# Performance work log

Hardware: AMD Instinct MI355X
Metric: run time of the kernel (lower is better)

## Reference

```python
import jax, jax.numpy as jnp
import numpy as np

B, C, H, W = 4, 256, 64, 64
RC = 32  # reduced channels = C // reduction


def setup_inputs() -> dict:
    key = jax.random.key(0)
    ks = jax.random.split(key, 5)
    return {
        "x": jax.random.normal(ks[0], (B, C, H, W), dtype=jnp.float32),
        "context": jax.random.normal(ks[1], (B, C, H, W), dtype=jnp.float32),
        "Wq": jax.random.normal(ks[2], (RC, C), dtype=jnp.float32) * 0.02,
        "bq": jnp.zeros((RC,), dtype=jnp.float32),
        "Wk": jax.random.normal(ks[3], (RC, C), dtype=jnp.float32) * 0.02,
        "bk": jnp.zeros((RC,), dtype=jnp.float32),
        "Wv": jax.random.normal(ks[4], (C, C), dtype=jnp.float32) * 0.02,
        "bv": jnp.zeros((C,), dtype=jnp.float32),
        "gamma": jnp.ones((1,), dtype=jnp.float32),
    }


def reference(x, context, Wq, bq, Wk, bk, Wv, bv, gamma):
    b, c, h, w = x.shape
    _, _, hc, wc = context.shape
    n, m = h * w, hc * wc
    xf = x.reshape(b, c, n)          # (B,C,N)
    cf = context.reshape(b, c, m)    # (B,C,M)
    # 1x1 conv projections == per-pixel linear
    q = jnp.einsum('rc,bcn->bnr', Wq, xf) + bq            # (B,N,RC)
    k = jnp.einsum('rc,bcm->brm', Wk, cf) + bk[:, None]   # (B,RC,M)
    v = jnp.einsum('dc,bcm->bdm', Wv, cf) + bv[:, None]   # (B,C,M)
    scale = 1.0 / jnp.sqrt(jnp.asarray(q.shape[-1], dtype=q.dtype))
    attn = jax.nn.softmax(jnp.einsum('bnr,brm->bnm', q, k) * scale, axis=-1)  # (B,N,M)
    out = jnp.einsum('bdm,bnm->bdn', v, attn).reshape(b, c, h, w)
    return gamma * out + x
```

## Files before the change

### kernel.cpp

```cpp
#include <hip/hip_runtime.h>
#include <hip/hip_bf16.h>


#define B_ 4
#define C_ 256
#define N_ 4096
#define M_ 4096
#define SCALE_ 0.17677669529663687f

typedef __bf16 bf16x8 __attribute__((ext_vector_type(8)));
typedef float f32x4 __attribute__((ext_vector_type(4)));
typedef float f32x16 __attribute__((ext_vector_type(16)));
typedef int i32x8 __attribute__((ext_vector_type(8)));

#define AS1 __attribute__((address_space(1)))
#define AS3 __attribute__((address_space(3)))

static __device__ __forceinline__ unsigned short f2bf(float f) {
    unsigned int u = __float_as_uint(f);
    return (unsigned short)((u + 0x7fffu + ((u >> 16) & 1u)) >> 16);
}
static __device__ __forceinline__ unsigned bfpk(float a, float b) {
    return (unsigned)f2bf(a) | ((unsigned)f2bf(b) << 16);
}

__global__ __launch_bounds__(256) void prep(
        const float* __restrict__ Wq, const float* __restrict__ Wk,
        const float* __restrict__ Wv, uint4* __restrict__ Wqf,
        uint4* __restrict__ Wkf, uint4* __restrict__ Wvf) {
    int bid = blockIdx.x, t = threadIdx.x;
    const float* W;
    uint4* dst;
    int frag;
    if (bid < 32)      { W = Wv; dst = Wvf; frag = (bid * 256 + t) >> 6; }
    else if (bid < 36) { W = Wq; dst = Wqf; frag = ((bid - 32) * 256 + t) >> 6; }
    else               { W = Wk; dst = Wkf; frag = ((bid - 36) * 256 + t) >> 6; }
    int lane = t & 63, low = lane & 15, q = lane >> 4;
    int fch = frag & 7, fr = frag >> 3;
    const float* wp = W + (size_t)(fr * 16 + low) * C_ + fch * 32 + q * 8;
    float4 w0 = *(const float4*)wp;
    float4 w1 = *(const float4*)(wp + 4);
    uint4 pk = {bfpk(w0.x, w0.y), bfpk(w0.z, w0.w),
                bfpk(w1.x, w1.y), bfpk(w1.z, w1.w)};
    dst[(size_t)frag * 64 + lane] = pk;
}

__global__ __launch_bounds__(256, 2) void fused_proj(
        const float* __restrict__ x, const float* __restrict__ ctx,
        const uint4* __restrict__ Wqf, const uint4* __restrict__ Wkf,
        const uint4* __restrict__ Wvf,
        const float* __restrict__ bq, const float* __restrict__ bk,
        const float* __restrict__ bv,
        unsigned short* __restrict__ Qf, unsigned short* __restrict__ Kf,
        unsigned char* __restrict__ Vf) {
    __shared__ unsigned short X[64][264];
    __shared__ unsigned short Pl[4][16 * 40];
    __shared__ unsigned char  Vw[4][16 * 40];

    int bid = blockIdx.x;
    bool isX = bid >= 256;
    int lb = bid & 255;
    int b = lb >> 6, pt64 = lb & 63;
    const float* __restrict__ in = (isX ? x : ctx) + (size_t)b * C_ * N_ + pt64 * 64;
    int t = threadIdx.x, wg = t >> 6, lane = t & 63;
    int low = lane & 15, q = lane >> 4;

    {
        int pL = lane;
        const float* s0 = in + pL;
#pragma unroll
        for (int ct = 0; ct < 4; ct++) {
            const float* s2 = s0 + (size_t)(ct * 64 + wg * 16) * N_;
            float v[16];
#pragma unroll
            for (int k = 0; k < 16; k++) v[k] = s2[(size_t)k * N_];
#pragma unroll
            for (int k = 0; k < 16; k += 2)
                *(unsigned*)&X[pL][ct * 64 + wg * 16 + k] = bfpk(v[k], v[k + 1]);
        }
    }
    __syncthreads();

    {
        const uint4* __restrict__ Wf = isX ? Wqf : Wkf;
        const float* __restrict__ bias = isX ? bq : bk;
        unsigned short* __restrict__ dst = isX ? Qf : Kf;
        bf16x8 xf[8];
#pragma unroll
        for (int ch = 0; ch < 8; ch++)
            xf[ch] = *(const bf16x8*)&X[wg * 16 + low][ch * 32 + q * 8];
        const f32x4 zero = {0.f, 0.f, 0.f, 0.f};
        f32x4 acc[2] = {zero, zero};
#pragma unroll
        for (int rt = 0; rt < 2; rt++)
#pragma unroll
            for (int ch = 0; ch < 8; ch++) {
                uint4 wv = Wf[(rt * 8 + ch) * 64 + lane];
                acc[rt] = __builtin_amdgcn_mfma_f32_16x16x32_bf16(
                    __builtin_bit_cast(bf16x8, wv), xf[ch], acc[rt], 0, 0, 0);
            }
        unsigned short* Pw = &Pl[wg][0];
#pragma unroll
        for (int rt = 0; rt < 2; rt++) {
            float b0 = bias[rt * 16 + q * 4 + 0], b1 = bias[rt * 16 + q * 4 + 1];
            float b2 = bias[rt * 16 + q * 4 + 2], b3 = bias[rt * 16 + q * 4 + 3];
            uint2 pk = {bfpk(acc[rt][0] + b0, acc[rt][1] + b1),
                        bfpk(acc[rt][2] + b2, acc[rt][3] + b3)};
            *(uint2*)(Pw + low * 40 + rt * 16 + q * 4) = pk;
        }
        uint4 frag = *(const uint4*)(Pw + low * 40 + q * 8);
        ((uint4*)dst)[((size_t)b * 256 + pt64 * 4 + wg) * 64 + lane] = frag;
    }

    if (!isX) {
        int mstep = wg >> 1, dh = wg & 1;
        bf16x8 vfr[2][8];
#pragma unroll
        for (int mt = 0; mt < 2; mt++)
#pragma unroll
            for (int ch = 0; ch < 8; ch++)
                vfr[mt][ch] = *(const bf16x8*)&X[mstep * 32 + mt * 16 + low][ch * 32 + q * 8];
        unsigned char* Vv = &Vw[wg][0];
        int msg = pt64 * 2 + mstep;
        const f32x4 zero = {0.f, 0.f, 0.f, 0.f};
#pragma unroll
        for (int dt8 = 0; dt8 < 8; dt8++) {
            int dt = dh * 8 + dt8;
            f32x4 a0 = zero, a1 = zero;
#pragma unroll
            for (int ch = 0; ch < 8; ch++) {
                uint4 wv = Wvf[(dt * 8 + ch) * 64 + lane];
                bf16x8 wfr = __builtin_bit_cast(bf16x8, wv);
                a0 = __builtin_amdgcn_mfma_f32_16x16x32_bf16(vfr[0][ch], wfr, a0, 0, 0, 0);
                a1 = __builtin_amdgcn_mfma_f32_16x16x32_bf16(vfr[1][ch], wfr, a1, 0, 0, 0);
            }
            float bb = bv[dt * 16 + low];
            unsigned w0 = __builtin_amdgcn_cvt_pk_fp8_f32(a0[0] + bb, a0[1] + bb, 0, false);
            w0 = __builtin_amdgcn_cvt_pk_fp8_f32(a0[2] + bb, a0[3] + bb, w0, true);
            unsigned w1 = __builtin_amdgcn_cvt_pk_fp8_f32(a1[0] + bb, a1[1] + bb, 0, false);
            w1 = __builtin_amdgcn_cvt_pk_fp8_f32(a1[2] + bb, a1[3] + bb, w1, true);
            *(unsigned*)(Vv + low * 40 + q * 4) = w0;
            *(unsigned*)(Vv + low * 40 + 16 + q * 4) = w1;
            uint2 fr = *(const uint2*)(Vv + low * 40 + q * 8);
            ((uint2*)Vf)[(((size_t)b * 128 + msg) * 16 + dt) * 64 + lane] = fr;
        }
    }
}

__global__ __launch_bounds__(512, 2) void attn(
        const unsigned short* __restrict__ Qf, const unsigned short* __restrict__ Kf,
        const unsigned char* __restrict__ Vf, const float* __restrict__ x,
        const float* __restrict__ gamma, float* __restrict__ out) {
    __shared__ __align__(16) unsigned char Pb[2][4][16 * 80];
    __shared__ float l_sh[64];
    __shared__ unsigned Ot[64 * 129];

    int bid = blockIdx.x;
    int xcd = bid & 7, tq = bid >> 3;
    int b = xcd >> 1;
    int g = ((xcd & 1) << 5) + tq;

    int wave = threadIdx.x >> 6, lane = threadIdx.x & 63;
    int q = lane >> 4, low = lane & 15;
    int hi = lane >> 5;
    int dsel = q & 1;
    int l31 = lane & 31;
    bool isQK = wave < 4;

    const uint4* Qp = (const uint4*)Qf;
    const uint4* Kp = (const uint4*)Kf + (size_t)b * 256 * 64;
    const uint2* Vq = (const uint2*)(Vf + (size_t)b * 1048576) + (size_t)hi * 1024 + low;
    int dt = wave * 2 + dsel;

    bf16x8 qa;
    if (isQK)
        qa = __builtin_bit_cast(bf16x8, Qp[(size_t)(b * 256 + g * 4 + wave) * 64 + lane]);

    f32x16 acc2[2];
    acc2[0] = (f32x16)(0.f);
    acc2[1] = (f32x16)(0.f);
    float lacc = 0.f;
    const f32x4 zero = {0.f, 0.f, 0.f, 0.f};

    uint4 kv[4];
    f32x4 s[4];
    if (isQK) {
#pragma unroll
        for (int u = 0; u < 4; u++)
            kv[u] = Kp[(size_t)u * 64 + lane];
#pragma unroll
        for (int u = 0; u < 4; u++)
            s[u] = __builtin_amdgcn_mfma_f32_16x16x32_bf16(
                __builtin_bit_cast(bf16x8, kv[u]), qa, zero, 0, 0, 0);
#pragma unroll
        for (int u = 0; u < 4; u++)
            kv[u] = Kp[(size_t)(4 + u) * 64 + lane];
        unsigned char* Pw = &Pb[0][wave][0];
#pragma unroll
        for (int u = 0; u < 4; u++) {
            float p0 = __expf(s[u][0] * SCALE_), p1 = __expf(s[u][1] * SCALE_);
            float p2 = __expf(s[u][2] * SCALE_), p3 = __expf(s[u][3] * SCALE_);
            lacc += p0 + p1 + p2 + p3;
            unsigned w = __builtin_amdgcn_cvt_pk_fp8_f32(p0, p1, 0, false);
            w = __builtin_amdgcn_cvt_pk_fp8_f32(p2, p3, w, true);
            *(unsigned*)(Pw + low * 80 + u * 16 + q * 4) = w;
        }
    }
    i32x8 vfc;
    {
        const uint2* Vs = Vq + (size_t)dt * 64;
        long* dqw = (long*)&vfc;
#pragma unroll
        for (int ss = 0; ss < 4; ss++)
            dqw[ss] = *(const long*)(Vs + ss * 16);
    }
    __syncthreads();

    for (int i = 0; i < 64; i++) {
        int cur = i & 1, nxt = cur ^ 1;
        bool haveNext = (i + 1 < 64);

        i32x8 vfn;
        if (haveNext) {
            const uint2* Vs = Vq + (size_t)(i + 1) * 2048 + dt * 64;
            long* dqw = (long*)&vfn;
#pragma unroll
            for (int ss = 0; ss < 4; ss++)
                dqw[ss] = *(const long*)(Vs + ss * 16);
        }

        if (isQK && haveNext) {
#pragma unroll
            for (int u = 0; u < 4; u++)
                s[u] = __builtin_amdgcn_mfma_f32_16x16x32_bf16(
                    __builtin_bit_cast(bf16x8, kv[u]), qa, zero, 0, 0, 0);
            if (i + 2 < 64) {
#pragma unroll
                for (int u = 0; u < 4; u++)
                    kv[u] = Kp[(size_t)((i + 2) * 4 + u) * 64 + lane];
            }
        }

        const unsigned char* Pr = &Pb[cur][0][0];
        __builtin_amdgcn_s_setprio(1);
#pragma unroll
        for (int tp = 0; tp < 2; tp++) {
            const unsigned char* pr = Pr + (tp * 2 + dsel) * 1280 + low * 80 + hi * 32;
            i32x8 pf;
            ((uint4*)&pf)[0] = *(const uint4*)pr;
            ((uint4*)&pf)[1] = *(const uint4*)(pr + 16);
            acc2[tp] = __builtin_amdgcn_mfma_scale_f32_32x32x64_f8f6f4(
                vfc, pf, acc2[tp], 0, 0, 0, 127, 0, 127);
        }
        __builtin_amdgcn_s_setprio(0);

        if (isQK && haveNext) {
            unsigned char* Pw = &Pb[nxt][wave][0];
#pragma unroll
            for (int u = 0; u < 4; u++) {
                float p0 = __expf(s[u][0] * SCALE_), p1 = __expf(s[u][1] * SCALE_);
                float p2 = __expf(s[u][2] * SCALE_), p3 = __expf(s[u][3] * SCALE_);
                lacc += p0 + p1 + p2 + p3;
                unsigned w = __builtin_amdgcn_cvt_pk_fp8_f32(p0, p1, 0, false);
                w = __builtin_amdgcn_cvt_pk_fp8_f32(p2, p3, w, true);
                *(unsigned*)(Pw + low * 80 + u * 16 + q * 4) = w;
            }
        }
        if (haveNext) vfc = vfn;
        __syncthreads();
    }

    if (isQK) {
        lacc += __shfl_xor(lacc, 16, 64);
        lacc += __shfl_xor(lacc, 32, 64);
        if (lane < 16)
            l_sh[wave * 16 + low] = lacc;
    }

#pragma unroll
    for (int tp = 0; tp < 2; tp++)
#pragma unroll
        for (int r = 0; r < 16; r += 2) {
            int col16 = wave * 16 + ((r >> 1) & 1) + 4 * (r >> 2) + 2 * hi;
            Ot[(tp * 32 + l31) * 129 + col16] = bfpk(acc2[tp][r], acc2[tp][r + 1]);
        }
    __syncthreads();

    {
        float gm = gamma[0];
        float rinv = gm / l_sh[lane];
        size_t nb = ((size_t)(b * 256 + wave * 32)) * 4096 + g * 64 + lane;
#pragma unroll 4
        for (int j = 0; j < 32; j++) {
            unsigned pk = Ot[lane * 129 + wave * 16 + (j >> 1)];
            unsigned bits = (j & 1) ? (pk & 0xffff0000u) : (pk << 16);
            float o = __uint_as_float(bits);
            size_t idx = nb + (size_t)j * 4096;
            out[idx] = o * rinv + x[idx];
        }
    }
}

extern "C" void kernel_launch(void* const* d_in, const int* in_sizes, int n_in,
                              void* d_out, int out_size, void* d_ws, size_t ws_size,
                              hipStream_t stream) {
    const float* x     = (const float*)d_in[0];
    const float* ctx   = (const float*)d_in[1];
    const float* Wq    = (const float*)d_in[2];
    const float* bq    = (const float*)d_in[3];
    const float* Wk    = (const float*)d_in[4];
    const float* bk    = (const float*)d_in[5];
    const float* Wv    = (const float*)d_in[6];
    const float* bv    = (const float*)d_in[7];
    const float* gamma = (const float*)d_in[8];
    float* out = (float*)d_out;

    unsigned short* Qf = (unsigned short*)d_ws;
    unsigned short* Kf = Qf + (size_t)B_ * N_ * 32;
    unsigned char*  Vf = (unsigned char*)(Kf + (size_t)B_ * M_ * 32);
    uint4* Wqf = (uint4*)(Vf + (size_t)B_ * M_ * C_);
    uint4* Wkf = Wqf + 16 * 64;
    uint4* Wvf = Wkf + 16 * 64;

    prep<<<40, 256, 0, stream>>>(Wq, Wk, Wv, Wqf, Wkf, Wvf);
    fused_proj<<<512, 256, 0, stream>>>(x, ctx, Wqf, Wkf, Wvf, bq, bk, bv, Qf, Kf, Vf);
    attn<<<256, 512, 0, stream>>>(Qf, Kf, Vf, x, gamma, out);
}
```

Before: 139.6 us.

## Halve attention query tile per block, double grid, use lighter barrier

Each attention block now handles 32 query rows instead of 64, so twice as many blocks are launched and launch bounds allow 4 blocks per CU. The QK work is split so that four waves each compute half the keys for one of two 16-query tiles, and the row sums are combined from two partial sums. A custom barrier waits only on LDS counters instead of using a full __syncthreads. The aim is better occupancy and latency hiding across 256 CUs, at the cost of reloading every V fragment twice as often overall and doing less MFMA work per barrier.

After: 142.2 us. Within noise of the previous version (+1.9%).

```diff
diff --git a/kernel.cpp b/kernel.cpp
--- a/kernel.cpp
+++ b/kernel.cpp
@@ -22,6 +22,11 @@
 }
 static __device__ __forceinline__ unsigned bfpk(float a, float b) {
     return (unsigned)f2bf(a) | ((unsigned)f2bf(b) << 16);
+}
+static __device__ __forceinline__ void p_barrier() {
+    asm volatile("s_waitcnt lgkmcnt(0)" ::: "memory");
+    __builtin_amdgcn_s_barrier();
+    asm volatile("" ::: "memory");
 }
 
 __global__ __launch_bounds__(256) void prep(
@@ -147,18 +152,18 @@
     }
 }
 
-__global__ __launch_bounds__(512, 2) void attn(
+__global__ __launch_bounds__(512, 4) void attn(
         const unsigned short* __restrict__ Qf, const unsigned short* __restrict__ Kf,
         const unsigned char* __restrict__ Vf, const float* __restrict__ x,
         const float* __restrict__ gamma, float* __restrict__ out) {
-    __shared__ __align__(16) unsigned char Pb[2][4][16 * 80];
-    __shared__ float l_sh[64];
-    __shared__ unsigned Ot[64 * 129];
+    __shared__ __align__(16) unsigned char Pb[2][2][16 * 80];
+    __shared__ float l_sh[2][32];
+    __shared__ unsigned Ot[32 * 129];
 
     int bid = blockIdx.x;
-    int xcd = bid & 7, tq = bid >> 3;
+    int xcd = bid & 7;
     int b = xcd >> 1;
-    int g = ((xcd & 1) << 5) + tq;
+    int g = ((xcd & 1) << 6) | (bid >> 3);
 
     int wave = threadIdx.x >> 6, lane = threadIdx.x & 63;
     int q = lane >> 4, low = lane & 15;
@@ -166,6 +171,8 @@
     int dsel = q & 1;
     int l31 = lane & 31;
     bool isQK = wave < 4;
+    int t = wave & 1;
+    int h = (wave >> 1) & 1;
 
     const uint4* Qp = (const uint4*)Qf;
     const uint4* Kp = (const uint4*)Kf + (size_t)b * 256 * 64;
@@ -174,36 +181,34 @@
 
     bf16x8 qa;
     if (isQK)
-        qa = __builtin_bit_cast(bf16x8, Qp[(size_t)(b * 256 + g * 4 + wave) * 64 + lane]);
-
-    f32x16 acc2[2];
-    acc2[0] = (f32x16)(0.f);
-    acc2[1] = (f32x16)(0.f);
+        qa = __builtin_bit_cast(bf16x8, Qp[(size_t)(b * 256 + g * 2 + t) * 64 + lane]);
+
+    f32x16 acc = (f32x16)(0.f);
     float lacc = 0.f;
     const f32x4 zero = {0.f, 0.f, 0.f, 0.f};
 
-    uint4 kv[4];
-    f32x4 s[4];
+    uint4 kv[2];
+    f32x4 s[2];
     if (isQK) {
 #pragma unroll
-        for (int u = 0; u < 4; u++)
-            kv[u] = Kp[(size_t)u * 64 + lane];
-#pragma unroll
-        for (int u = 0; u < 4; u++)
+        for (int u = 0; u < 2; u++)
+            kv[u] = Kp[(size_t)(h * 2 + u) * 64 + lane];
+#pragma unroll
+        for (int u = 0; u < 2; u++)
             s[u] = __builtin_amdgcn_mfma_f32_16x16x32_bf16(
                 __builtin_bit_cast(bf16x8, kv[u]), qa, zero, 0, 0, 0);
 #pragma unroll
-        for (int u = 0; u < 4; u++)
-            kv[u] = Kp[(size_t)(4 + u) * 64 + lane];
-        unsigned char* Pw = &Pb[0][wave][0];
-#pragma unroll
-        for (int u = 0; u < 4; u++) {
+        for (int u = 0; u < 2; u++)
+            kv[u] = Kp[(size_t)(4 + h * 2 + u) * 64 + lane];
+        unsigned char* Pw = &Pb[0][t][0];
+#pragma unroll
+        for (int u = 0; u < 2; u++) {
             float p0 = __expf(s[u][0] * SCALE_), p1 = __expf(s[u][1] * SCALE_);
             float p2 = __expf(s[u][2] * SCALE_), p3 = __expf(s[u][3] * SCALE_);
             lacc += p0 + p1 + p2 + p3;
             unsigned w = __builtin_amdgcn_cvt_pk_fp8_f32(p0, p1, 0, false);
             w = __builtin_amdgcn_cvt_pk_fp8_f32(p2, p3, w, true);
-            *(unsigned*)(Pw + low * 80 + u * 16 + q * 4) = w;
+            *(unsigned*)(Pw + low * 80 + h * 32 + u * 16 + q * 4) = w;
         }
     }
     i32x8 vfc;
@@ -214,7 +219,7 @@
         for (int ss = 0; ss < 4; ss++)
             dqw[ss] = *(const long*)(Vs + ss * 16);
     }
-    __syncthreads();
+    p_barrier();
 
     for (int i = 0; i < 64; i++) {
         int cur = i & 1, nxt = cur ^ 1;
@@ -231,68 +236,66 @@
 
         if (isQK && haveNext) {
 #pragma unroll
-            for (int u = 0; u < 4; u++)
+            for (int u = 0; u < 2; u++)
                 s[u] = __builtin_amdgcn_mfma_f32_16x16x32_bf16(
                     __builtin_bit_cast(bf16x8, kv[u]), qa, zero, 0, 0, 0);
             if (i + 2 < 64) {
 #pragma unroll
-                for (int u = 0; u < 4; u++)
-                    kv[u] = Kp[(size_t)((i + 2) * 4 + u) * 64 + lane];
+                for (int u = 0; u < 2; u++)
+                    kv[u] = Kp[(size_t)((i + 2) * 4 + h * 2 + u) * 64 + lane];
             }
         }
 
-        const unsigned char* Pr = &Pb[cur][0][0];
-        __builtin_amdgcn_s_setprio(1);
-#pragma unroll
-        for (int tp = 0; tp < 2; tp++) {
-            const unsigned char* pr = Pr + (tp * 2 + dsel) * 1280 + low * 80 + hi * 32;
+        {
+            const unsigned char* pr = &Pb[cur][0][0] + dsel * 1280 + low * 80 + hi * 32;
             i32x8 pf;
             ((uint4*)&pf)[0] = *(const uint4*)pr;
             ((uint4*)&pf)[1] = *(const uint4*)(pr + 16);
-            acc2[tp] = __builtin_amdgcn_mfma_scale_f32_32x32x64_f8f6f4(
-                vfc, pf, acc2[tp], 0, 0, 0, 127, 0, 127);
-        }
-        __builtin_amdgcn_s_setprio(0);
+            __builtin_amdgcn_s_setprio(1);
+            acc = __builtin_amdgcn_mfma_scale_f32_32x32x64_f8f6f4(
+                vfc, pf, acc, 0, 0, 0, 127, 0, 127);
+            __builtin_amdgcn_s_setprio(0);
+        }
 
         if (isQK && haveNext) {
-            unsigned char* Pw = &Pb[nxt][wave][0];
-#pragma unroll
-            for (int u = 0; u < 4; u++) {
+            unsigned char* Pw = &Pb[nxt][t][0];
+#pragma unroll
+            for (int u = 0; u < 2; u++) {
                 float p0 = __expf(s[u][0] * SCALE_), p1 = __expf(s[u][1] * SCALE_);
                 float p2 = __expf(s[u][2] * SCALE_), p3 = __expf(s[u][3] * SCALE_);
                 lacc += p0 + p1 + p2 + p3;
                 unsigned w = __builtin_amdgcn_cvt_pk_fp8_f32(p0, p1, 0, false);
                 w = __builtin_amdgcn_cvt_pk_fp8_f32(p2, p3, w, true);
-                *(unsigned*)(Pw + low * 80 + u * 16 + q * 4) = w;
+                *(unsigned*)(Pw + low * 80 + h * 32 + u * 16 + q * 4) = w;
             }
         }
         if (haveNext) vfc = vfn;
-        __syncthreads();
+        p_barrier();
     }
 
     if (isQK) {
         lacc += __shfl_xor(lacc, 16, 64);
         lacc += __shfl_xor(lacc, 32, 64);
         if (lane < 16)
-            l_sh[wave * 16 + low] = lacc;
-    }
-
-#pragma unroll
-    for (int tp = 0; tp < 2; tp++)
-#pragma unroll
-        for (int r = 0; r < 16; r += 2) {
-            int col16 = wave * 16 + ((r >> 1) & 1) + 4 * (r >> 2) + 2 * hi;
-            Ot[(tp * 32 + l31) * 129 + col16] = bfpk(acc2[tp][r], acc2[tp][r + 1]);
-        }
+            l_sh[h][t * 16 + low] = lacc;
+    }
+
+#pragma unroll
+    for (int r = 0; r < 16; r += 2) {
+        int col16 = wave * 16 + ((r >> 1) & 1) + 4 * (r >> 2) + 2 * hi;
+        Ot[l31 * 129 + col16] = bfpk(acc[r], acc[r + 1]);
+    }
     __syncthreads();
 
     {
         float gm = gamma[0];
-        float rinv = gm / l_sh[lane];
-        size_t nb = ((size_t)(b * 256 + wave * 32)) * 4096 + g * 64 + lane;
+        float rinv = gm / (l_sh[0][l31] + l_sh[1][l31]);
+        int dh = lane >> 5;
+        size_t nb = ((size_t)(b * 256 + wave * 32 + dh * 16)) * 4096
+                    + (size_t)g * 32 + l31;
 #pragma unroll 4
-        for (int j = 0; j < 32; j++) {
-            unsigned pk = Ot[lane * 129 + wave * 16 + (j >> 1)];
+        for (int j = 0; j < 16; j++) {
+            unsigned pk = Ot[l31 * 129 + wave * 16 + dh * 8 + (j >> 1)];
             unsigned bits = (j & 1) ? (pk & 0xffff0000u) : (pk << 16);
             float o = __uint_as_float(bits);
             size_t idx = nb + (size_t)j * 4096;
@@ -324,5 +327,5 @@
 
     prep<<<40, 256, 0, stream>>>(Wq, Wk, Wv, Wqf, Wkf, Wvf);
     fused_proj<<<512, 256, 0, stream>>>(x, ctx, Wqf, Wkf, Wvf, bq, bk, bv, Qf, Kf, Vf);
-    attn<<<256, 512, 0, stream>>>(Qf, Kf, Vf, x, gamma, out);
-}
+    attn<<<512, 512, 0, stream>>>(Qf, Kf, Vf, x, gamma, out);
+}
```

## Stream K tiles into LDS asynchronously and use contiguous V fragment loads

Applied to the files above, without the earlier changes.

K tiles are now prefetched with global_load_lds directly into a double-buffered LDS area two iterations ahead, and the QK waves read them from LDS rather than holding them in registers. The V fragment layout written by the prep kernel is permuted so each lane's 32-byte V fragment is contiguous and can be loaded with a single vector load. The __syncthreads is replaced by a manual vmcnt wait plus s_barrier so outstanding V loads can stay in flight across the barrier. The aim is to cut register pressure and global load latency in the attention loop, at the cost of relying on hand-placed waitcnt counts being correct.

Result: slower. 152.1 us (+9.0%).

```diff
diff --git a/kernel.cpp b/kernel.cpp
--- a/kernel.cpp
+++ b/kernel.cpp
@@ -22,6 +22,15 @@
 }
 static __device__ __forceinline__ unsigned bfpk(float a, float b) {
     return (unsigned)f2bf(a) | ((unsigned)f2bf(b) << 16);
+}
+static __device__ __forceinline__ void gload_lds16(const void* g, void* l) {
+    __builtin_amdgcn_global_load_lds((const AS1 unsigned int*)g,
+                                     (AS3 unsigned int*)l, 16, 0, 0);
+}
+static __device__ __forceinline__ void p_barrier() {
+    asm volatile("s_waitcnt lgkmcnt(0)" ::: "memory");
+    __builtin_amdgcn_s_barrier();
+    asm volatile("" ::: "memory");
 }
 
 __global__ __launch_bounds__(256) void prep(
@@ -122,6 +131,7 @@
                 vfr[mt][ch] = *(const bf16x8*)&X[mstep * 32 + mt * 16 + low][ch * 32 + q * 8];
         unsigned char* Vv = &Vw[wg][0];
         int msg = pt64 * 2 + mstep;
+        int perm = (lane & 15) * 4 + (lane >> 4);
         const f32x4 zero = {0.f, 0.f, 0.f, 0.f};
 #pragma unroll
         for (int dt8 = 0; dt8 < 8; dt8++) {
@@ -142,7 +152,7 @@
             *(unsigned*)(Vv + low * 40 + q * 4) = w0;
             *(unsigned*)(Vv + low * 40 + 16 + q * 4) = w1;
             uint2 fr = *(const uint2*)(Vv + low * 40 + q * 8);
-            ((uint2*)Vf)[(((size_t)b * 128 + msg) * 16 + dt) * 64 + lane] = fr;
+            ((uint2*)Vf)[(((size_t)b * 128 + msg) * 16 + dt) * 64 + perm] = fr;
         }
     }
 }
@@ -152,6 +162,7 @@
         const unsigned char* __restrict__ Vf, const float* __restrict__ x,
         const float* __restrict__ gamma, float* __restrict__ out) {
     __shared__ __align__(16) unsigned char Pb[2][4][16 * 80];
+    __shared__ __align__(16) unsigned char Kl[2][4096];
     __shared__ float l_sh[64];
     __shared__ unsigned Ot[64 * 129];
 
@@ -168,9 +179,11 @@
     bool isQK = wave < 4;
 
     const uint4* Qp = (const uint4*)Qf;
-    const uint4* Kp = (const uint4*)Kf + (size_t)b * 256 * 64;
-    const uint2* Vq = (const uint2*)(Vf + (size_t)b * 1048576) + (size_t)hi * 1024 + low;
+    const unsigned char* Kb = (const unsigned char*)(Kf + (size_t)b * 256 * 32 * 2 * 4);
+    Kb = (const unsigned char*)Kf + (size_t)b * 262144;
     int dt = wave * 2 + dsel;
+    const unsigned char* Vq = Vf + (size_t)b * 1048576
+                              + (size_t)hi * 8192 + (size_t)dt * 512 + (size_t)low * 32;
 
     bf16x8 qa;
     if (isQK)
@@ -187,14 +200,17 @@
     if (isQK) {
 #pragma unroll
         for (int u = 0; u < 4; u++)
-            kv[u] = Kp[(size_t)u * 64 + lane];
+            kv[u] = *(const uint4*)(Kb + (size_t)(u * 64 + lane) * 16);
+        gload_lds16(Kb + 4096 + wave * 1024 + lane * 16,
+                    &Kl[0][wave * 1024 + lane * 16]);
+    }
+    asm volatile("" ::: "memory");
+    i32x8 vfc = *(const i32x8*)Vq;
+    if (isQK) {
 #pragma unroll
         for (int u = 0; u < 4; u++)
             s[u] = __builtin_amdgcn_mfma_f32_16x16x32_bf16(
                 __builtin_bit_cast(bf16x8, kv[u]), qa, zero, 0, 0, 0);
-#pragma unroll
-        for (int u = 0; u < 4; u++)
-            kv[u] = Kp[(size_t)(4 + u) * 64 + lane];
         unsigned char* Pw = &Pb[0][wave][0];
 #pragma unroll
         for (int u = 0; u < 4; u++) {
@@ -206,39 +222,29 @@
             *(unsigned*)(Pw + low * 80 + u * 16 + q * 4) = w;
         }
     }
-    i32x8 vfc;
-    {
-        const uint2* Vs = Vq + (size_t)dt * 64;
-        long* dqw = (long*)&vfc;
-#pragma unroll
-        for (int ss = 0; ss < 4; ss++)
-            dqw[ss] = *(const long*)(Vs + ss * 16);
-    }
-    __syncthreads();
+    asm volatile("s_waitcnt vmcnt(2)" ::: "memory");
+    p_barrier();
 
     for (int i = 0; i < 64; i++) {
         int cur = i & 1, nxt = cur ^ 1;
-        bool haveNext = (i + 1 < 64);
+        bool hn = (i + 1 < 64);
+
+        if (isQK && i + 2 < 64)
+            gload_lds16(Kb + (size_t)(i + 2) * 4096 + wave * 1024 + lane * 16,
+                        &Kl[nxt][wave * 1024 + lane * 16]);
+        asm volatile("" ::: "memory");
 
         i32x8 vfn;
-        if (haveNext) {
-            const uint2* Vs = Vq + (size_t)(i + 1) * 2048 + dt * 64;
-            long* dqw = (long*)&vfn;
-#pragma unroll
-            for (int ss = 0; ss < 4; ss++)
-                dqw[ss] = *(const long*)(Vs + ss * 16);
-        }
-
-        if (isQK && haveNext) {
+        if (hn) vfn = *(const i32x8*)(Vq + (size_t)(i + 1) * 16384);
+
+        if (isQK && hn) {
+#pragma unroll
+            for (int u = 0; u < 4; u++)
+                kv[u] = *(const uint4*)&Kl[cur][u * 1024 + lane * 16];
 #pragma unroll
             for (int u = 0; u < 4; u++)
                 s[u] = __builtin_amdgcn_mfma_f32_16x16x32_bf16(
                     __builtin_bit_cast(bf16x8, kv[u]), qa, zero, 0, 0, 0);
-            if (i + 2 < 64) {
-#pragma unroll
-                for (int u = 0; u < 4; u++)
-                    kv[u] = Kp[(size_t)((i + 2) * 4 + u) * 64 + lane];
-            }
         }
 
         const unsigned char* Pr = &Pb[cur][0][0];
@@ -254,7 +260,7 @@
         }
         __builtin_amdgcn_s_setprio(0);
 
-        if (isQK && haveNext) {
+        if (isQK && hn) {
             unsigned char* Pw = &Pb[nxt][wave][0];
 #pragma unroll
             for (int u = 0; u < 4; u++) {
@@ -266,8 +272,9 @@
                 *(unsigned*)(Pw + low * 80 + u * 16 + q * 4) = w;
             }
         }
-        if (haveNext) vfc = vfn;
-        __syncthreads();
+        if (hn) vfc = vfn;
+        asm volatile("s_waitcnt vmcnt(2)" ::: "memory");
+        p_barrier();
     }
 
     if (isQK) {
```

## Double-buffer V fragments two steps ahead and use a barrier that skips the vmcnt wait

Applied to the files above, without the earlier changes.

The main loop now prefetches V fragments two iterations ahead into two alternating register sets (vA/vB), unrolled by two. The exp/P-write work for the next tile moves ahead of the PV MFMAs. __syncthreads is replaced with a barrier that waits only on LDS counters (lgkmcnt), so global V and K loads stay in flight across barriers. The aim is to hide global-load latency and stop barriers from draining vmcnt, at the cost of more registers and a subtler ordering that relies on the P double buffer.

Result: slower. 147.9 us (+6.0%).

```diff
diff --git a/kernel.cpp b/kernel.cpp
--- a/kernel.cpp
+++ b/kernel.cpp
@@ -22,6 +22,11 @@
 }
 static __device__ __forceinline__ unsigned bfpk(float a, float b) {
     return (unsigned)f2bf(a) | ((unsigned)f2bf(b) << 16);
+}
+static __device__ __forceinline__ void p_barrier() {
+    asm volatile("s_waitcnt lgkmcnt(0)" ::: "memory");
+    __builtin_amdgcn_s_barrier();
+    asm volatile("" ::: "memory");
 }
 
 __global__ __launch_bounds__(256) void prep(
@@ -184,6 +189,18 @@
 
     uint4 kv[4];
     f32x4 s[4];
+    i32x8 vA, vB;
+
+    {
+        long* dqw = (long*)&vA;
+#pragma unroll
+        for (int ss = 0; ss < 4; ss++)
+            dqw[ss] = *(const long*)(Vq + dt * 64 + ss * 16);
+        long* dqx = (long*)&vB;
+#pragma unroll
+        for (int ss = 0; ss < 4; ss++)
+            dqx[ss] = *(const long*)(Vq + 2048 + dt * 64 + ss * 16);
+    }
     if (isQK) {
 #pragma unroll
         for (int u = 0; u < 4; u++)
@@ -206,56 +223,20 @@
             *(unsigned*)(Pw + low * 80 + u * 16 + q * 4) = w;
         }
     }
-    i32x8 vfc;
-    {
-        const uint2* Vs = Vq + (size_t)dt * 64;
-        long* dqw = (long*)&vfc;
-#pragma unroll
-        for (int ss = 0; ss < 4; ss++)
-            dqw[ss] = *(const long*)(Vs + ss * 16);
-    }
-    __syncthreads();
-
-    for (int i = 0; i < 64; i++) {
-        int cur = i & 1, nxt = cur ^ 1;
-        bool haveNext = (i + 1 < 64);
-
-        i32x8 vfn;
-        if (haveNext) {
-            const uint2* Vs = Vq + (size_t)(i + 1) * 2048 + dt * 64;
-            long* dqw = (long*)&vfn;
-#pragma unroll
-            for (int ss = 0; ss < 4; ss++)
-                dqw[ss] = *(const long*)(Vs + ss * 16);
-        }
-
-        if (isQK && haveNext) {
+    p_barrier();
+
+    auto step = [&](int j, i32x8& Vuse) {
+        if (isQK && j + 1 < 64) {
 #pragma unroll
             for (int u = 0; u < 4; u++)
                 s[u] = __builtin_amdgcn_mfma_f32_16x16x32_bf16(
                     __builtin_bit_cast(bf16x8, kv[u]), qa, zero, 0, 0, 0);
-            if (i + 2 < 64) {
+            if (j + 2 < 64) {
 #pragma unroll
                 for (int u = 0; u < 4; u++)
-                    kv[u] = Kp[(size_t)((i + 2) * 4 + u) * 64 + lane];
-            }
-        }
-
-        const unsigned char* Pr = &Pb[cur][0][0];
-        __builtin_amdgcn_s_setprio(1);
-#pragma unroll
-        for (int tp = 0; tp < 2; tp++) {
-            const unsigned char* pr = Pr + (tp * 2 + dsel) * 1280 + low * 80 + hi * 32;
-            i32x8 pf;
-            ((uint4*)&pf)[0] = *(const uint4*)pr;
-            ((uint4*)&pf)[1] = *(const uint4*)(pr + 16);
-            acc2[tp] = __builtin_amdgcn_mfma_scale_f32_32x32x64_f8f6f4(
-                vfc, pf, acc2[tp], 0, 0, 0, 127, 0, 127);
-        }
-        __builtin_amdgcn_s_setprio(0);
-
-        if (isQK && haveNext) {
-            unsigned char* Pw = &Pb[nxt][wave][0];
+                    kv[u] = Kp[(size_t)((j + 2) * 4 + u) * 64 + lane];
+            }
+            unsigned char* Pw = &Pb[(j + 1) & 1][wave][0];
 #pragma unroll
             for (int u = 0; u < 4; u++) {
                 float p0 = __expf(s[u][0] * SCALE_), p1 = __expf(s[u][1] * SCALE_);
@@ -266,8 +247,35 @@
                 *(unsigned*)(Pw + low * 80 + u * 16 + q * 4) = w;
             }
         }
-        if (haveNext) vfc = vfn;
-        __syncthreads();
+
+        {
+            const unsigned char* Pr = &Pb[j & 1][0][0];
+            __builtin_amdgcn_s_setprio(1);
+#pragma unroll
+            for (int tp = 0; tp < 2; tp++) {
+                const unsigned char* pr = Pr + (tp * 2 + dsel) * 1280 + low * 80 + hi * 32;
+                i32x8 pf;
+                ((uint4*)&pf)[0] = *(const uint4*)pr;
+                ((uint4*)&pf)[1] = *(const uint4*)(pr + 16);
+                acc2[tp] = __builtin_amdgcn_mfma_scale_f32_32x32x64_f8f6f4(
+                    Vuse, pf, acc2[tp], 0, 0, 0, 127, 0, 127);
+            }
+            __builtin_amdgcn_s_setprio(0);
+        }
+
+        if (j + 2 < 64) {
+            const uint2* Vs = Vq + (size_t)(j + 2) * 2048;
+            long* dqw = (long*)&Vuse;
+#pragma unroll
+            for (int ss = 0; ss < 4; ss++)
+                dqw[ss] = *(const long*)(Vs + dt * 64 + ss * 16);
+        }
+        p_barrier();
+    };
+
+    for (int i = 0; i < 64; i += 2) {
+        step(i, vA);
+        step(i + 1, vB);
     }
 
     if (isQK) {
```
